# Optimization experiments

Measured on AMD Instinct MI355X. Metric: run time of the kernel, lower is better.

## Reference

```python
import jax, jax.numpy as jnp
import numpy as np

B, N, C = 4, 2048, 81
IMG_W, IMG_H = 1024.0, 800.0
SCORE_THRESH = 0.05
NMS_THRESH = 0.5
DETS_PER_IMG = 100
BBOX_XFORM_CLIP = float(np.log(1000.0 / 16.0))
WX, WY, WW, WH = 10.0, 10.0, 5.0, 5.0


def _make_boxes(key, n):
    k1, k2, k3, k4 = jax.random.split(key, 4)
    x1 = jax.random.uniform(k1, (n,)) * (IMG_W - 60.0)
    y1 = jax.random.uniform(k2, (n,)) * (IMG_H - 60.0)
    w = 10.0 + jax.random.uniform(k3, (n,)) * 300.0
    h = 10.0 + jax.random.uniform(k4, (n,)) * 300.0
    return jnp.stack([x1, y1, jnp.minimum(x1 + w, IMG_W - 1.0), jnp.minimum(y1 + h, IMG_H - 1.0)], axis=-1)


def setup_inputs() -> dict:
    key = jax.random.key(0)
    k1, k2, k3, k4 = jax.random.split(key, 4)
    return {
        "class_logits": jax.random.normal(k1, (B * N, C), jnp.float32),
        "box_regression": jax.random.normal(k2, (B * N, C * 8), jnp.float32) * 0.5,
        "left_proposals": _make_boxes(k3, B * N),
        "right_proposals": _make_boxes(k4, B * N),
    }


def decode(rel, boxes):
    widths = boxes[:, 2] - boxes[:, 0] + 1.0
    heights = boxes[:, 3] - boxes[:, 1] + 1.0
    ctr_x = boxes[:, 0] + 0.5 * widths
    ctr_y = boxes[:, 1] + 0.5 * heights
    dx = rel[:, 0::4] / WX
    dy = rel[:, 1::4] / WY
    dw = jnp.minimum(rel[:, 2::4] / WW, BBOX_XFORM_CLIP)
    dh = jnp.minimum(rel[:, 3::4] / WH, BBOX_XFORM_CLIP)
    pcx = dx * widths[:, None] + ctr_x[:, None]
    pcy = dy * heights[:, None] + ctr_y[:, None]
    pw = jnp.exp(dw) * widths[:, None]
    ph = jnp.exp(dh) * heights[:, None]
    x1 = pcx - 0.5 * pw
    y1 = pcy - 0.5 * ph
    x2 = pcx + 0.5 * pw - 1.0
    y2 = pcy + 0.5 * ph - 1.0
    return jnp.stack([x1, y1, x2, y2], axis=-1)  # [M, C, 4]


def clip_boxes(b):
    x1 = jnp.clip(b[..., 0], 0.0, IMG_W - 1.0)
    y1 = jnp.clip(b[..., 1], 0.0, IMG_H - 1.0)
    x2 = jnp.clip(b[..., 2], 0.0, IMG_W - 1.0)
    y2 = jnp.clip(b[..., 3], 0.0, IMG_H - 1.0)
    return jnp.stack([x1, y1, x2, y2], axis=-1)


def pairwise_iou(b):
    area = jnp.clip(b[:, 2] - b[:, 0] + 1.0, 0.0) * jnp.clip(b[:, 3] - b[:, 1] + 1.0, 0.0)
    lt = jnp.maximum(b[:, None, :2], b[None, :, :2])
    rb = jnp.minimum(b[:, None, 2:], b[None, :, 2:])
    wh = jnp.clip(rb - lt + 1.0, 0.0)
    inter = wh[..., 0] * wh[..., 1]
    return inter / jnp.maximum(area[:, None] + area[None, :] - inter, 1e-6)


def nms_keep(boxes, scores):
    # greedy NMS -> boolean keep mask (fixed shape)
    n = scores.shape[0]
    order = jnp.argsort(-scores)
    iou = pairwise_iou(boxes[order])
    idx = jnp.arange(n)
    def body(i, keep):
        sup = (iou[i] > NMS_THRESH) & keep[i] & (idx > i)
        return keep & (~sup)
    keep = jax.lax.fori_loop(0, n, body, jnp.ones((n,), bool))
    return jnp.zeros((n,), bool).at[order].set(keep)


def _per_image(prob, lb, rb):
    # prob [N,C], lb/rb [N,C,4]
    labels = jnp.argmax(prob, axis=-1)
    ar = jnp.arange(prob.shape[0])
    score = prob[ar, labels]
    lbox = lb[ar, labels]
    rbox = rb[ar, labels]
    valid = (labels >= 1) & (score > SCORE_THRESH)
    s = jnp.where(valid, score, -jnp.inf)
    keep = nms_keep(lbox, s) & nms_keep(rbox, s) & valid
    ms = jnp.where(keep, score, -jnp.inf)
    kth = jax.lax.top_k(ms, DETS_PER_IMG)[0][-1]
    keep = keep & (ms >= kth)
    return lbox, rbox, score, keep


def reference(class_logits, box_regression, left_proposals, right_proposals):
    prob = jax.nn.softmax(class_logits, axis=-1)  # [B*N, C]
    reg = box_regression.reshape(-1, C, 8)
    lb = clip_boxes(decode(reg[:, :, :4].reshape(-1, C * 4), left_proposals))
    rb = clip_boxes(decode(reg[:, :, 4:].reshape(-1, C * 4), right_proposals))
    prob = prob.reshape(B, N, C)
    lb = lb.reshape(B, N, C, 4)
    rb = rb.reshape(B, N, C, 4)
    lbox, rbox, score, keep = jax.vmap(_per_image)(prob, lb, rb)
    m = keep[..., None].astype(score.dtype)
    out = jnp.concatenate([lbox * m, rbox * m, jnp.where(keep, score, 0.0)[..., None]], axis=-1)
    return out  # [B, N, 9]
```

## Files before the change

kernel.cpp:

```cpp
#include <hip/hip_runtime.h>
#include <math.h>

#define NPROP 2048
#define NIMG 4
#define NCLS 81
#define REGW 648
#define SCORE_THRESH 0.05f
#define NMS_T 0.5f
#define DETS 100
#define XC 1023.0f
#define YC 799.0f
#define BBOX_CLIP 4.135166556742356f
#define NBIN 8192
#define SEL 320
#define MAXC 512
#define WRD 8
#define TRIP 2560

typedef unsigned long long u64;

__device__ __forceinline__ float areaf(float4 v) {
  return fmaxf(v.z - v.x + 1.0f, 0.0f) * fmaxf(v.w - v.y + 1.0f, 0.0f);
}
__device__ __forceinline__ bool iou_gt(float4 a, float aa, float4 b, float ba) {
  float ix1 = fmaxf(a.x, b.x), iy1 = fmaxf(a.y, b.y);
  float ix2 = fminf(a.z, b.z), iy2 = fminf(a.w, b.w);
  float iw = fmaxf(ix2 - ix1 + 1.0f, 0.0f);
  float ih = fmaxf(iy2 - iy1 + 1.0f, 0.0f);
  float inter = iw * ih;
  return inter > NMS_T * fmaxf(aa + ba - inter, 1e-6f);
}
__device__ __forceinline__ float score_from_v(unsigned v) {
  unsigned uu = ~v;
  unsigned bits = (uu & 0x80000000u) ? (uu & 0x7fffffffu) : ~uu;
  return __uint_as_float(bits);
}
__device__ __forceinline__ float4 decode_math(float4 rr, float4 P) {
  float w  = P.z - P.x + 1.0f;
  float h  = P.w - P.y + 1.0f;
  float cx = P.x + 0.5f * w;
  float cy = P.y + 0.5f * h;
  float dx = rr.x / 10.0f;
  float dy = rr.y / 10.0f;
  float dw = fminf(rr.z / 5.0f, BBOX_CLIP);
  float dh = fminf(rr.w / 5.0f, BBOX_CLIP);
  float pcx = dx * w + cx;
  float pcy = dy * h + cy;
  float pw = expf(dw) * w;
  float ph = expf(dh) * h;
  float4 o;
  o.x = fminf(fmaxf(pcx - 0.5f * pw, 0.0f), XC);
  o.y = fminf(fmaxf(pcy - 0.5f * ph, 0.0f), YC);
  o.z = fminf(fmaxf(pcx + 0.5f * pw - 1.0f, 0.0f), XC);
  o.w = fminf(fmaxf(pcy + 0.5f * ph - 1.0f, 0.0f), YC);
  return o;
}
__device__ __forceinline__ float4 decode_side(const float* __restrict__ reg,
                                              const float4* __restrict__ props,
                                              int grow, int ci, int isR) {
  const float4 rr = *(const float4*)(reg + (size_t)grow * REGW + ci * 8 + isR * 4);
  return decode_math(rr, props[grow]);
}

__global__ __launch_bounds__(256) void score_kernel(
    const float* __restrict__ logits,
    unsigned* __restrict__ v32G, unsigned short* __restrict__ ci16G,
    int* __restrict__ doneG, float* __restrict__ out) {
  int row  = blockIdx.x * 4 + (threadIdx.x >> 6);
  int lane = threadIdx.x & 63;
  if (blockIdx.x == 0 && threadIdx.x < NIMG) doneG[threadIdx.x] = 0;
  if (blockIdx.x < 72) {
    int g = blockIdx.x * 256 + threadIdx.x;
    ((float4*)out)[g] = make_float4(0.f, 0.f, 0.f, 0.f);
  }
  const float* lr = logits + (size_t)row * NCLS;
  float a = lr[lane];
  float b = (lane < NCLS - 64) ? lr[lane + 64] : -INFINITY;
  float v; int ci;
  if (b > a) { v = b; ci = lane + 64; } else { v = a; ci = lane; }
  for (int o = 32; o; o >>= 1) {
    float ov = __shfl_xor(v, o);
    int   oc = __shfl_xor(ci, o);
    if (ov > v || (ov == v && oc < ci)) { v = ov; ci = oc; }
  }
  float e = expf(a - v) + ((lane < NCLS - 64) ? expf(b - v) : 0.0f);
  for (int o = 32; o; o >>= 1) e += __shfl_xor(e, o);
  if (lane == 0) {
    float score = 1.0f / e;
    unsigned vv = 0xFFFFFFFFu;
    if (ci >= 1 && score > SCORE_THRESH) {
      unsigned uu = __float_as_uint(score);
      uu = (uu & 0x80000000u) ? ~uu : (uu | 0x80000000u);
      vv = ~uu;
    }
    v32G[row]  = vv;
    ci16G[row] = (unsigned short)ci;
  }
}

struct P2S {
  int hist[NBIN];
  u64 keys[MAXC];
  unsigned short ssort[MAXC];
  unsigned svs[MAXC];
  float4 bx[MAXC];
  u64 mat[TRIP];
  int rnk[MAXC];
  int wsum[16];
  int Ts, cnts, ovf;
};

struct SN {
  u64 keys[NPROP];
  unsigned short sidx[NPROP];
  unsigned v32s[NPROP];
  float4 bxL[MAXC], bxR[MAXC];
  float  arL[MAXC], arR[MAXC];
  u64 keepbL[NPROP / 64], keepbR[NPROP / 64];
  u64 rowmL[64], rowmR[64];
  float4 cbL[64], cbR[64];
  float  cbLa[64], cbRa[64];
  u64 aL, aR;
  int cnt, prevCount, done, ccL, ccR, needFB;
  unsigned kthV;
};

__device__ __forceinline__ float4 get_sboxN(SN* S, const float* reg,
                                            const float4* lp4, const float4* rp4,
                                            const unsigned short* ci16G,
                                            int b, int pos, int isR) {
  if (pos < MAXC) return isR ? S->bxR[pos] : S->bxL[pos];
  int row = S->sidx[pos];
  int grow = b * NPROP + row;
  return decode_side(reg, isR ? rp4 : lp4, grow, ci16G[grow], isR);
}

__global__ __launch_bounds__(1024) void nms_fused_kernel(
    const unsigned* __restrict__ v32G, const unsigned short* __restrict__ ci16G,
    const float* __restrict__ reg, const float* __restrict__ lp,
    const float* __restrict__ rp,
    float4* __restrict__ bxRG, u64* __restrict__ keepRG,
    int* __restrict__ doneG, float* __restrict__ out) {
  constexpr unsigned SMEM = (sizeof(P2S) > sizeof(SN)) ? sizeof(P2S) : sizeof(SN);
  __shared__ __align__(16) char smemRaw[SMEM];
  P2S& P = *reinterpret_cast<P2S*>(smemRaw);
  SN&  S = *reinterpret_cast<SN*>(smemRaw);

  int b = blockIdx.x >> 1, side = blockIdx.x & 1;
  int tid = threadIdx.x, ln = tid & 63, w = tid >> 6;
  const unsigned* v32 = v32G + b * NPROP;
  const unsigned short* ci16 = ci16G + b * NPROP;

  unsigned vA0 = v32[tid], vA1 = v32[tid + 1024];
  unsigned cA0 = ci16[tid], cA1 = ci16[tid + 1024];
  if (tid == 0) { P.Ts = NBIN - 1; P.cnts = 0; P.ovf = 0; }
  for (int i = tid; i < NBIN; i += 1024) P.hist[i] = 0;
  if (tid < MAXC) P.rnk[tid] = 0;
  __syncthreads();
  if (vA0 != 0xFFFFFFFFu) atomicAdd(&P.hist[vA0 >> 19], 1);
  if (vA1 != 0xFFFFFFFFu) atomicAdd(&P.hist[vA1 >> 19], 1);
  __syncthreads();
  {
    int base = tid * 8;
    int c[8]; int acc = 0;
#pragma unroll
    for (int k = 0; k < 8; ++k) { acc += P.hist[base + k]; c[k] = acc; }
    int tot = acc, v = tot;
#pragma unroll
    for (int o = 1; o < 64; o <<= 1) { int n = __shfl_up(v, o); if (ln >= o) v += n; }
    if (ln == 63) P.wsum[w] = v;
    __syncthreads();
    if (tid < 16) {
      int x = P.wsum[tid];
#pragma unroll
      for (int o = 1; o < 16; o <<= 1) { int n = __shfl_up(x, o); if (tid >= o) x += n; }
      P.wsum[tid] = x;
    }
    __syncthreads();
    int incl = ((w > 0) ? P.wsum[w - 1] : 0) + v;
    int off = incl - tot;
    int prev = off;
#pragma unroll
    for (int k = 0; k < 8; ++k) {
      int cur = off + c[k];
      if (cur >= SEL && prev < SEL) P.Ts = base + k;
      prev = cur;
    }
  }
  __syncthreads();
  int T = P.Ts, nvTot = P.wsum[15];
  {
    unsigned vv[2] = {vA0, vA1};
    unsigned cc[2] = {cA0, cA1};
#pragma unroll
    for (int it = 0; it < 2; ++it) {
      int p = tid + it * 1024;
      unsigned v = vv[it];
      bool cand = (v != 0xFFFFFFFFu) && ((int)(v >> 19) <= T);
      u64 mb = __ballot(cand);
      int lpos = (int)__popcll(mb & ((1ull << ln) - 1ull));
      int wb = 0;
      if (ln == 0 && mb) wb = atomicAdd(&P.cnts, (int)__popcll(mb));
      wb = __shfl(wb, 0);
      if (cand) {
        int dst = wb + lpos;
        if (dst < MAXC)
          P.keys[dst] = ((u64)v << 32) | ((u64)p << 21) | ((u64)cc[it] << 14);
        else P.ovf = 1;
      }
    }
  }
  __syncthreads();
  int C1 = P.cnts;
  bool skipSel = (C1 > MAXC) || P.ovf;
  u64 A[WRD];

  if (!skipSel) {
    float4 rrD, ppD;
    unsigned myv = 0; int myp = 0;
    bool hasKey = (tid < C1);
    if (hasKey) {
      u64 k = P.keys[tid];
      myv = (unsigned)(k >> 32);
      myp = (int)((k >> 21) & 0x7FF);
      int myci = (int)((k >> 14) & 0x7F);
      int grow = b * NPROP + myp;
      ppD = ((const float4*)(side ? rp : lp))[grow];
      rrD = *(const float4*)(reg + (size_t)grow * REGW + myci * 8 + side * 4);
    }
    {
      int i = tid & (MAXC - 1), h = tid >> 9;
      if (i < C1) {
        u64 ki = P.keys[i];
        int half = (C1 + 1) >> 1;
        int jlo = h ? half : 0, jhi = h ? C1 : half;
        int r = 0;
#pragma unroll 4
        for (int j = jlo; j < jhi; ++j) r += (P.keys[j] < ki) ? 1 : 0;
        atomicAdd(&P.rnk[i], r);
      }
    }
    __syncthreads();
    if (hasKey) {
      int R = P.rnk[tid];
      float4 B = decode_math(rrD, ppD);
      P.bx[R] = B;
      P.ssort[R] = (unsigned short)myp;
      P.svs[R] = myv;
      if (side) bxRG[b * MAXC + R] = B;
    }
    if (tid >= C1 && tid < MAXC) P.bx[tid] = make_float4(0.f, 0.f, 0.f, 0.f);
    __syncthreads();

    int WRDu = (C1 + 63) >> 6;
    {
      int rb = w & 7, part = w >> 3;
      int r = rb * 64 + ln;
      float4 rbx = P.bx[r];
      float  rar = areaf(rbx);
      int tb = 0;
      for (int k = 0; k < rb; ++k) tb += ((8 - k) | 1);
      int Sw = (8 - rb) | 1;
      u64* myrow = &P.mat[tb * 64 + ln * Sw];
      for (int cw = rb + part; cw < WRDu; cw += 2) {
        u64 m = 0;
        const float4* cp = &P.bx[cw * 64];
#pragma unroll 8
        for (int c = 0; c < 64; ++c) {
          float4 cb = cp[c];
          float car = areaf(cb);
          if (iou_gt(rbx, rar, cb, car)) m |= (1ull << c);
        }
        if (cw == rb) m &= ~((2ull << ln) - 1ull);
        myrow[cw - rb] = m;
      }
    }
    __syncthreads();

    if (w == 0) {
#pragma unroll
      for (int t = 0; t < WRD; ++t) {
        int b0 = t * 64;
        A[t] = (C1 >= b0 + 64) ? ~0ull : (C1 > b0 ? ((1ull << (C1 - b0)) - 1ull) : 0ull);
      }
      int tbase = 0;
#pragma unroll
      for (int wb = 0; wb < WRD; ++wb) {
        if (wb * 64 < C1) {
          const int Sw = (8 - wb) | 1;
          const u64* rowp = &P.mat[tbase];
          u64 aw = A[wb];
#pragma unroll
          for (int g = 0; g < 4; ++g) {
            u64 d[16];
#pragma unroll
            for (int k = 0; k < 16; ++k) d[k] = rowp[(g * 16 + k) * Sw];
#pragma unroll
            for (int k = 0; k < 16; ++k) {
              u64 msk = 0ull - ((aw >> (g * 16 + k)) & 1ull);
              aw &= ~(msk & d[k]);
            }
          }
          A[wb] = aw;
          bool alive = (aw >> ln) & 1ull;
#pragma unroll
          for (int t = wb + 1; t < WRD; ++t) {
            if (t * 64 < C1) {
              u64 x = alive ? rowp[ln * Sw + (t - wb)] : 0ull;
#pragma unroll
              for (int o = 1; o < 64; o <<= 1)
                x |= __shfl_xor((unsigned long long)x, o);
              A[t] &= ~x;
            }
          }
        }
        tbase += 64 * ((8 - wb) | 1);
      }
      if (ln == 0 && side == 1) {
        u64* kG = keepRG + b * WRD;
#pragma unroll
        for (int t = 0; t < WRD; ++t)
          if (t * 64 < C1) kG[t] = A[t];
      }
    }
  }
  __syncthreads();

  if (side == 1) {
    if (tid == 0) {
      __threadfence();
      __hip_atomic_store(&doneG[b], 1, __ATOMIC_RELEASE, __HIP_MEMORY_SCOPE_AGENT);
    }
    return;
  }
  if (tid == 0) {
    while (__hip_atomic_load(&doneG[b], __ATOMIC_ACQUIRE,
                             __HIP_MEMORY_SCOPE_AGENT) == 0)
      __builtin_amdgcn_s_sleep(2);
    __threadfence();
  }
  __syncthreads();

  float* ob = out + (size_t)b * NPROP * 9;
  int C1e = skipSel ? 0 : C1;
  if (w == 0) {
    int before = 0;
    unsigned kth = 0;
    for (int wb = 0; wb * 64 < C1e; ++wb) {
      u64 m = A[wb] & keepRG[b * WRD + wb];
      int pos = wb * 64 + ln;
      bool bit = (m >> ln) & 1ull;
      int rank = before + (int)__popcll(m & ((1ull << ln) - 1ull));
      unsigned vv = P.svs[pos];
      u64 selm = __ballot(bit && rank == DETS - 1);
      if (selm) kth = __shfl(vv, __ffsll(selm) - 1);
      bool qual = bit && (rank < DETS || vv == kth);
      if (qual) {
        int row = P.ssort[pos];
        float4 L = P.bx[pos];
        float4 R4 = bxRG[b * MAXC + pos];
        float* orow = ob + row * 9;
        orow[0]=L.x; orow[1]=L.y; orow[2]=L.z; orow[3]=L.w;
        orow[4]=R4.x; orow[5]=R4.y; orow[6]=R4.z; orow[7]=R4.w;
        orow[8]=score_from_v(vv);
      }
      before += (int)__popcll(m);
    }
    if (ln == 0) {
      S.needFB = (before < DETS && nvTot > C1e) ? 1 : 0;
      S.cnt = 0; S.prevCount = 0; S.done = 0; S.kthV = 0u;
    }
  }
  __syncthreads();
  if (!S.needFB) return;

  const float4* lp4 = (const float4*)lp;
  const float4* rp4 = (const float4*)rp;
  float4* ob4 = (float4*)ob;
  float4 z4 = make_float4(0.f, 0.f, 0.f, 0.f);
  for (int i = tid; i < NPROP * 9 / 4; i += 1024) ob4[i] = z4;
  for (int p = tid; p < NPROP; p += 1024) {
    unsigned v = v32G[b * NPROP + p];
    S.v32s[p] = v;
    bool cand = (v != 0xFFFFFFFFu);
    u64 mb = __ballot(cand);
    int lpos = (int)__popcll(mb & ((1ull << ln) - 1ull));
    int wb = 0;
    if (ln == 0 && mb) wb = atomicAdd(&S.cnt, (int)__popcll(mb));
    wb = __shfl(wb, 0);
    if (cand) S.keys[wb + lpos] = ((u64)v << 16) | (unsigned)p;
  }
  __syncthreads();
  int C2 = S.cnt;
  int CbEnd = (C2 + 63) & ~63;
  {
    int i0 = tid, i1 = tid + 1024;
    u64 k0 = (i0 < C2) ? S.keys[i0] : ~0ull;
    u64 k1 = (i1 < C2) ? S.keys[i1] : ~0ull;
    int r0 = 0, r1 = 0;
#pragma unroll 4
    for (int j = 0; j < C2; ++j) {
      u64 kj = S.keys[j];
      r0 += (kj < k0) ? 1 : 0;
      r1 += (kj < k1) ? 1 : 0;
    }
    if (i0 < C2) S.sidx[r0] = (unsigned short)(k0 & 0xFFFFull);
    if (i1 < C2) S.sidx[r1] = (unsigned short)(k1 & 0xFFFFull);
  }
  for (int i = C2 + tid; i < CbEnd; i += 1024) S.sidx[i] = 0;
  for (int wd = tid; wd < NPROP / 64; wd += 1024) {
    int b0 = wd << 6;
    u64 mf = 0ull;
    if (C2 >= b0 + 64) mf = ~0ull;
    else if (C2 > b0)  mf = (1ull << (C2 - b0)) - 1ull;
    S.keepbL[wd] = mf; S.keepbR[wd] = mf;
  }
  __syncthreads();
  {
    int lim = min(CbEnd, MAXC);
    for (int i = tid; i < lim; i += 1024) {
      if (i < C2) {
        int row = S.sidx[i];
        int grow = b * NPROP + row;
        int ci = ci16G[grow];
        float4 L = decode_side(reg, lp4, grow, ci, 0);
        float4 R = decode_side(reg, rp4, grow, ci, 1);
        S.bxL[i] = L; S.arL[i] = areaf(L);
        S.bxR[i] = R; S.arR[i] = areaf(R);
      } else {
        S.bxL[i] = z4; S.arL[i] = 1.0f;
        S.bxR[i] = z4; S.arR[i] = 1.0f;
      }
    }
  }
  __syncthreads();
  for (int base = 0; base < CbEnd; base += 64) {
    {
      int isR = (w >= 8);
      float4 cbx = get_sboxN(&S, reg, lp4, rp4, ci16G, b, base + ln, isR);
      float car = (base + ln < MAXC) ? (isR ? S.arR[base + ln] : S.arL[base + ln])
                                     : areaf(cbx);
      int w8 = w & 7;
#pragma unroll
      for (int k = 0; k < 8; ++k) {
        int row = w8 * 8 + k;
        float4 rbx;
        rbx.x = __shfl(cbx.x, row); rbx.y = __shfl(cbx.y, row);
        rbx.z = __shfl(cbx.z, row); rbx.w = __shfl(cbx.w, row);
        float rar = __shfl(car, row);
        bool bit = (ln > row) && iou_gt(rbx, rar, cbx, car);
        u64 bal = __ballot(bit);
        if (ln == 0) { if (isR) S.rowmR[row] = bal; else S.rowmL[row] = bal; }
      }
    }
    __syncthreads();
    if (tid < 128) {
      int isR = (tid >= 64);
      u64* km = isR ? S.keepbR : S.keepbL;
      u64* rm = isR ? S.rowmR  : S.rowmL;
      u64 a = km[base >> 6];
#pragma unroll
      for (int j = 0; j < 64; ++j)
        a &= ~((0ull - ((a >> j) & 1ull)) & rm[j]);
      if (ln == 0) {
        km[base >> 6] = a;
        if (isR) { S.aR = a; S.ccR = __popcll(a); }
        else     { S.aL = a; S.ccL = __popcll(a); }
      }
      if ((a >> ln) & 1ull) {
        int pos = __popcll(a & ((1ull << ln) - 1ull));
        float4 v = get_sboxN(&S, reg, lp4, rp4, ci16G, b, base + ln, isR);
        if (isR) { S.cbR[pos] = v; S.cbRa[pos] = areaf(v); }
        else     { S.cbL[pos] = v; S.cbLa[pos] = areaf(v); }
      }
    }
    __syncthreads();
    if (w == 0) {
      u64 m = S.aL & S.aR;
      int before = S.prevCount;
      bool bit = (m >> ln) & 1ull;
      int rank = before + (int)__popcll(m & ((1ull << ln) - 1ull));
      int row = S.sidx[base + ln];
      unsigned vv = S.v32s[row];
      u64 selm = __ballot(bit && rank == DETS - 1);
      unsigned keffV = S.kthV;
      if (selm) keffV = __shfl(vv, __ffsll(selm) - 1);
      bool qual = bit && (rank < DETS || vv == keffV);
      if (qual) {
        float4 L = get_sboxN(&S, reg, lp4, rp4, ci16G, b, base + ln, 0);
        float4 R = get_sboxN(&S, reg, lp4, rp4, ci16G, b, base + ln, 1);
        float s = score_from_v(vv);
        float* orow = ob + row * 9;
        orow[0]=L.x; orow[1]=L.y; orow[2]=L.z; orow[3]=L.w;
        orow[4]=R.x; orow[5]=R.y; orow[6]=R.z; orow[7]=R.w;
        orow[8]=s;
      }
      if (ln == 0) {
        if (selm) S.kthV = keffV;
        int nc = before + (int)__popcll(m);
        S.prevCount = nc;
        if (nc >= DETS) {
          int nxt = base + 64;
          bool cont = false;
          if (nxt < C2) cont = (S.v32s[S.sidx[nxt]] == keffV);
          if (!cont) S.done = 1;
        }
      }
    } else {
      int cL = S.ccL, cR = S.ccR;
      if ((cL | cR) != 0) {
        for (int p = base + 64 + (tid - 64); p < CbEnd; p += 960) {
          float4 mbL = get_sboxN(&S, reg, lp4, rp4, ci16G, b, p, 0);
          float al = (p < MAXC) ? S.arL[p] : areaf(mbL);
          bool supL = false;
          for (int q = 0; q < cL; ++q)
            supL = supL || iou_gt(mbL, al, S.cbL[q], S.cbLa[q]);
          if (supL) atomicAnd(&S.keepbL[p >> 6], ~(1ull << (p & 63)));
          float4 mbR = get_sboxN(&S, reg, lp4, rp4, ci16G, b, p, 1);
          float ar_ = (p < MAXC) ? S.arR[p] : areaf(mbR);
          bool supR = false;
          for (int q = 0; q < cR; ++q)
            supR = supR || iou_gt(mbR, ar_, S.cbR[q], S.cbRa[q]);
          if (supR) atomicAnd(&S.keepbR[p >> 6], ~(1ull << (p & 63)));
        }
      }
    }
    __syncthreads();
    if (S.done) break;
  }
}

extern "C" void kernel_launch(void* const* d_in, const int* in_sizes, int n_in,
                              void* d_out, int out_size, void* d_ws, size_t ws_size,
                              hipStream_t stream) {
  const float* logits = (const float*)d_in[0];
  const float* reg    = (const float*)d_in[1];
  const float* lprop  = (const float*)d_in[2];
  const float* rprop  = (const float*)d_in[3];
  float* out = (float*)d_out;

  char* ws = (char*)d_ws;
  unsigned*       v32G   = (unsigned*)(ws + 0);
  unsigned short* ci16G  = (unsigned short*)(ws + 32768);
  float4*         bxRG   = (float4*)(ws + 49152);
  u64*            keepRG = (u64*)(ws + 81920);
  int*            doneG  = (int*)(ws + 82176);

  score_kernel<<<NIMG * NPROP / 4, 256, 0, stream>>>(logits, v32G, ci16G,
                                                     doneG, out);
  nms_fused_kernel<<<2 * NIMG, 1024, 0, stream>>>(v32G, ci16G, reg, lprop, rprop,
                                                  bxRG, keepRG, doneG, out);
}
```

Baseline: 118.1 us.

## Refine top-k threshold with second-level histogram and restructure candidate ranking

Adds a second 1024-bin histogram pass over the threshold bin when the first-level selection would admit too many candidates. This tightens the candidate set toward SEL, so the later sort, decode and IoU-matrix stages handle fewer boxes. The rank computation changes from 1024 threads doing half-range counts with atomics to 256 threads each ranking two keys over the full range with direct stores. The refinement costs extra block-wide syncs and scans, and the new ranking runs on fewer threads with a longer loop.

```diff
diff --git a/kernel.cpp b/kernel.cpp
--- a/kernel.cpp
+++ b/kernel.cpp
@@ -12,7 +12,9 @@
 #define YC 799.0f
 #define BBOX_CLIP 4.135166556742356f
 #define NBIN 8192
+#define NBIN2 1024
 #define SEL 320
+#define SELSLACK 32
 #define MAXC 512
 #define WRD 8
 #define TRIP 2560
@@ -107,7 +109,7 @@
   u64 mat[TRIP];
   int rnk[MAXC];
   int wsum[16];
-  int Ts, cnts, ovf;
+  int Ts, T2s, cnts, ovf;
 };
 
 struct SN {
@@ -153,9 +155,8 @@
 
   unsigned vA0 = v32[tid], vA1 = v32[tid + 1024];
   unsigned cA0 = ci16[tid], cA1 = ci16[tid + 1024];
-  if (tid == 0) { P.Ts = NBIN - 1; P.cnts = 0; P.ovf = 0; }
+  if (tid == 0) { P.Ts = NBIN - 1; P.T2s = NBIN2 - 1; P.cnts = 0; P.ovf = 0; }
   for (int i = tid; i < NBIN; i += 1024) P.hist[i] = 0;
-  if (tid < MAXC) P.rnk[tid] = 0;
   __syncthreads();
   if (vA0 != 0xFFFFFFFFu) atomicAdd(&P.hist[vA0 >> 19], 1);
   if (vA1 != 0xFFFFFFFFu) atomicAdd(&P.hist[vA1 >> 19], 1);
@@ -185,10 +186,43 @@
       int cur = off + c[k];
       if (cur >= SEL && prev < SEL) P.Ts = base + k;
       prev = cur;
+      P.hist[base + k] = cur;
     }
   }
   __syncthreads();
   int T = P.Ts, nvTot = P.wsum[15];
+  int nb = (T > 0) ? P.hist[T - 1] : 0;
+  int nt = P.hist[T] - nb;
+  bool doRef = (nb + nt > SEL + SELSLACK);
+  __syncthreads();
+  int T2 = NBIN2 - 1;
+  if (doRef) {
+    P.hist[tid] = 0;
+    __syncthreads();
+    if (vA0 != 0xFFFFFFFFu && (int)(vA0 >> 19) == T)
+      atomicAdd(&P.hist[(vA0 >> 9) & (NBIN2 - 1)], 1);
+    if (vA1 != 0xFFFFFFFFu && (int)(vA1 >> 19) == T)
+      atomicAdd(&P.hist[(vA1 >> 9) & (NBIN2 - 1)], 1);
+    __syncthreads();
+    int need = SEL - nb;
+    int x = P.hist[tid];
+    int v = x;
+#pragma unroll
+    for (int o = 1; o < 64; o <<= 1) { int n = __shfl_up(v, o); if (ln >= o) v += n; }
+    if (ln == 63) P.wsum[w] = v;
+    __syncthreads();
+    if (tid < 16) {
+      int y = P.wsum[tid];
+#pragma unroll
+      for (int o = 1; o < 16; o <<= 1) { int n = __shfl_up(y, o); if (tid >= o) y += n; }
+      P.wsum[tid] = y;
+    }
+    __syncthreads();
+    int incl = ((w > 0) ? P.wsum[w - 1] : 0) + v;
+    if (incl >= need && incl - x < need) P.T2s = tid;
+    __syncthreads();
+    T2 = P.T2s;
+  }
   {
     unsigned vv[2] = {vA0, vA1};
     unsigned cc[2] = {cA0, cA1};
@@ -196,7 +230,9 @@
     for (int it = 0; it < 2; ++it) {
       int p = tid + it * 1024;
       unsigned v = vv[it];
-      bool cand = (v != 0xFFFFFFFFu) && ((int)(v >> 19) <= T);
+      int bin = (int)(v >> 19);
+      bool cand = (v != 0xFFFFFFFFu) &&
+                  (bin < T || (bin == T && (int)((v >> 9) & (NBIN2 - 1)) <= T2));
       u64 mb = __ballot(cand);
       int lpos = (int)__popcll(mb & ((1ull << ln) - 1ull));
       int wb = 0;
@@ -228,17 +264,19 @@
       ppD = ((const float4*)(side ? rp : lp))[grow];
       rrD = *(const float4*)(reg + (size_t)grow * REGW + myci * 8 + side * 4);
     }
-    {
-      int i = tid & (MAXC - 1), h = tid >> 9;
-      if (i < C1) {
-        u64 ki = P.keys[i];
-        int half = (C1 + 1) >> 1;
-        int jlo = h ? half : 0, jhi = h ? C1 : half;
-        int r = 0;
+    if (tid < 256) {
+      int i0 = tid, i1 = tid + 256;
+      u64 k0 = (i0 < C1) ? P.keys[i0] : ~0ull;
+      u64 k1 = (i1 < C1) ? P.keys[i1] : ~0ull;
+      int r0 = 0, r1 = 0;
 #pragma unroll 4
-        for (int j = jlo; j < jhi; ++j) r += (P.keys[j] < ki) ? 1 : 0;
-        atomicAdd(&P.rnk[i], r);
-      }
+      for (int j = 0; j < C1; ++j) {
+        u64 kj = P.keys[j];
+        r0 += (kj < k0) ? 1 : 0;
+        r1 += (kj < k1) ? 1 : 0;
+      }
+      if (i0 < C1) P.rnk[i0] = r0;
+      if (i1 < C1) P.rnk[i1] = r1;
     }
     __syncthreads();
     if (hasKey) {
```

Result: slower. 122.5 us (+3.8%).

## Build NMS IoU mask via wave ballots and rank keys without atomics

Applied to the files above, without the earlier changes.

The IoU suppression matrix is now computed with each lane holding one column box per word and looping over rows, using a wave ballot to form each 64-bit mask, instead of each lane looping serially over 64 columns. The sort-rank step now has 256 threads each ranking two keys with a direct store, replacing the split-half atomicAdd scheme and removing the rnk zeroing. The histogram clear uses vectorized int4 stores. The ballot approach spreads work across lanes, but it adds per-row broadcast reads and a serial row loop, and the rank step uses fewer threads over a longer loop.

```diff
diff --git a/kernel.cpp b/kernel.cpp
--- a/kernel.cpp
+++ b/kernel.cpp
@@ -154,8 +154,8 @@
   unsigned vA0 = v32[tid], vA1 = v32[tid + 1024];
   unsigned cA0 = ci16[tid], cA1 = ci16[tid + 1024];
   if (tid == 0) { P.Ts = NBIN - 1; P.cnts = 0; P.ovf = 0; }
-  for (int i = tid; i < NBIN; i += 1024) P.hist[i] = 0;
-  if (tid < MAXC) P.rnk[tid] = 0;
+  for (int i = tid; i < NBIN / 4; i += 1024)
+    ((int4*)P.hist)[i] = make_int4(0, 0, 0, 0);
   __syncthreads();
   if (vA0 != 0xFFFFFFFFu) atomicAdd(&P.hist[vA0 >> 19], 1);
   if (vA1 != 0xFFFFFFFFu) atomicAdd(&P.hist[vA1 >> 19], 1);
@@ -228,17 +228,19 @@
       ppD = ((const float4*)(side ? rp : lp))[grow];
       rrD = *(const float4*)(reg + (size_t)grow * REGW + myci * 8 + side * 4);
     }
-    {
-      int i = tid & (MAXC - 1), h = tid >> 9;
-      if (i < C1) {
-        u64 ki = P.keys[i];
-        int half = (C1 + 1) >> 1;
-        int jlo = h ? half : 0, jhi = h ? C1 : half;
-        int r = 0;
+    if (tid < 256) {
+      int i0 = tid, i1 = tid + 256;
+      u64 k0 = (i0 < C1) ? P.keys[i0] : ~0ull;
+      u64 k1 = (i1 < C1) ? P.keys[i1] : ~0ull;
+      int r0 = 0, r1 = 0;
 #pragma unroll 4
-        for (int j = jlo; j < jhi; ++j) r += (P.keys[j] < ki) ? 1 : 0;
-        atomicAdd(&P.rnk[i], r);
-      }
+      for (int j = 0; j < C1; ++j) {
+        u64 kj = P.keys[j];
+        r0 += (kj < k0) ? 1 : 0;
+        r1 += (kj < k1) ? 1 : 0;
+      }
+      if (i0 < C1) P.rnk[i0] = r0;
+      if (i1 < C1) P.rnk[i1] = r1;
     }
     __syncthreads();
     if (hasKey) {
@@ -255,24 +257,44 @@
     int WRDu = (C1 + 63) >> 6;
     {
       int rb = w & 7, part = w >> 3;
-      int r = rb * 64 + ln;
-      float4 rbx = P.bx[r];
-      float  rar = areaf(rbx);
-      int tb = 0;
-      for (int k = 0; k < rb; ++k) tb += ((8 - k) | 1);
-      int Sw = (8 - rb) | 1;
-      u64* myrow = &P.mat[tb * 64 + ln * Sw];
-      for (int cw = rb + part; cw < WRDu; cw += 2) {
-        u64 m = 0;
-        const float4* cp = &P.bx[cw * 64];
-#pragma unroll 8
-        for (int c = 0; c < 64; ++c) {
-          float4 cb = cp[c];
-          float car = areaf(cb);
-          if (iou_gt(rbx, rar, cb, car)) m |= (1ull << c);
+      int K = WRDu - rb;
+      if (K > 0 && rb * 64 < C1) {
+        float4 cbx[8]; float car[8];
+#pragma unroll
+        for (int k = 0; k < 8; ++k) {
+          if (k < K) {
+            cbx[k] = P.bx[(rb + k) * 64 + ln];
+            car[k] = areaf(cbx[k]);
+          }
         }
-        if (cw == rb) m &= ~((2ull << ln) - 1ull);
-        myrow[cw - rb] = m;
+        u64 rw[8];
+#pragma unroll
+        for (int k = 0; k < 8; ++k) rw[k] = 0ull;
+        int tb = 0;
+        for (int kk = 0; kk < rb; ++kk) tb += ((8 - kk) | 1);
+        int Sw = (8 - rb) | 1;
+        int r0 = part * 32;
+        int rlim = C1 - rb * 64; if (rlim > 64) rlim = 64;
+        for (int j = 0; j < 32; ++j) {
+          int rl = r0 + j;
+          if (rl >= rlim) break;
+          float4 rbx = P.bx[rb * 64 + rl];
+          float rar = areaf(rbx);
+#pragma unroll
+          for (int k = 0; k < 8; ++k) {
+            if (k < K) {
+              u64 bal = __ballot(iou_gt(rbx, rar, cbx[k], car[k]));
+              if (k == 0) bal &= ~((2ull << rl) - 1ull);
+              rw[k] = (ln == rl) ? bal : rw[k];
+            }
+          }
+        }
+        if (ln >= r0 && ln < r0 + 32 && ln < rlim) {
+          u64* myrow = &P.mat[tb * 64 + ln * Sw];
+#pragma unroll
+          for (int k = 0; k < 8; ++k)
+            if (k < K) myrow[k] = rw[k];
+        }
       }
     }
     __syncthreads();
```

New measurement: 118.2 us. Within noise of the previous version (+0.1%).
